# Performance work log

Measured on AMD Instinct MI355X. Metric: run time of the kernel, lower is better.

The kernel has to match this reference:

```python
import jax, jax.numpy as jnp
import numpy as np

B, N, E, H, HEADS = 4, 10000, 160000, 128, 4
NEG_SLOPE = 0.2  # PyG GATConv default
LN_EPS = 1e-5


def setup_inputs() -> dict:
    key = jax.random.key(0)
    ks = jax.random.split(key, 24)
    inp = {}
    inp["node_embeddings"] = jax.random.normal(ks[0], (B, N, H), dtype=jnp.float32)
    inp["src_index"] = jax.random.randint(ks[1], (B, E), 0, N)
    inp["tgt_index"] = jax.random.randint(ks[2], (B, E), 0, N)
    sc = 1.0 / np.sqrt(H)
    for i in range(3):
        j = 3 + 3 * i
        inp[f"W{i+1}"] = jax.random.normal(ks[j], (H, HEADS * H), dtype=jnp.float32) * sc
        inp[f"att_src{i+1}"] = jax.random.normal(ks[j + 1], (HEADS, H), dtype=jnp.float32) * sc
        inp[f"att_dst{i+1}"] = jax.random.normal(ks[j + 2], (HEADS, H), dtype=jnp.float32) * sc
        inp[f"bias{i+1}"] = jnp.zeros((H,), dtype=jnp.float32)
    inp["ln1_g"] = jnp.ones((H,), dtype=jnp.float32)
    inp["ln1_b"] = jnp.zeros((H,), dtype=jnp.float32)
    inp["ln2_g"] = jnp.ones((H,), dtype=jnp.float32)
    inp["ln2_b"] = jnp.zeros((H,), dtype=jnp.float32)
    return inp


def _layer_norm(x, g, b):
    mu = jnp.mean(x, axis=-1, keepdims=True)
    var = jnp.mean((x - mu) ** 2, axis=-1, keepdims=True)
    return (x - mu) * jax.lax.rsqrt(var + LN_EPS) * g + b


def _gat(x, src, tgt, W, a_s, a_d, b):
    # x: [N, H]; src/tgt: [E'] (self-loops already appended). eval mode -> no dropout.
    h = (x @ W).reshape(N, HEADS, H)               # [N, heads, H]
    e_src = jnp.einsum('nhc,hc->nh', h, a_s)       # [N, heads]
    e_dst = jnp.einsum('nhc,hc->nh', h, a_d)
    e = jax.nn.leaky_relu(e_src[src] + e_dst[tgt], NEG_SLOPE)  # [E', heads]
    m = jax.ops.segment_max(e, tgt, num_segments=N)            # per-target max
    ex = jnp.exp(e - m[tgt])
    s = jax.ops.segment_sum(ex, tgt, num_segments=N)
    alpha = ex / s[tgt]                                        # [E', heads]
    out = jax.ops.segment_sum(alpha[:, :, None] * h[src], tgt, num_segments=N)
    return out.mean(axis=1) + b                                # concat=False -> head mean


def reference(node_embeddings, src_index, tgt_index,
              W1, att_src1, att_dst1, bias1,
              W2, att_src2, att_dst2, bias2,
              W3, att_src3, att_dst3, bias3,
              ln1_g, ln1_b, ln2_g, ln2_b):
    loop = jnp.arange(N, dtype=src_index.dtype)

    def one_graph(x, src, tgt):
        s = jnp.concatenate([src, loop])   # GATConv add_self_loops=True (default)
        t = jnp.concatenate([tgt, loop])
        m = _gat(x, s, t, W1, att_src1, att_dst1, bias1)
        m = jax.nn.relu(_layer_norm(m, ln1_g, ln1_b))
        m = _gat(m, s, t, W2, att_src2, att_dst2, bias2)
        m = jax.nn.relu(_layer_norm(m, ln2_g, ln2_b))
        m = _gat(m, s, t, W3, att_src3, att_dst3, bias3)
        return m

    return jax.vmap(one_graph)(node_embeddings, src_index, tgt_index)
```

## Files before the change

kernel.cpp:

```cpp
#include <hip/hip_runtime.h>
#include <hip/hip_bf16.h>
#include <cstdint>
#include <cstddef>

#define B_ 4
#define N_ 10000
#define E_ 160000
#define H_ 128
#define HEADS_ 4
#define HH_ 512
#define NROWS (B_*N_)

typedef __attribute__((ext_vector_type(8))) short bf16x8;
typedef __attribute__((ext_vector_type(4))) float f32x4;
typedef __attribute__((ext_vector_type(2))) float f32x2;

__device__ __forceinline__ float lrelu(float x){ return x > 0.f ? x : 0.2f*x; }
__device__ __forceinline__ unsigned short f2b(float f){
  unsigned int u = __builtin_bit_cast(unsigned int, f);
  unsigned int r = (u + 0x7fffu + ((u >> 16) & 1u)) >> 16;
  return (unsigned short)r;
}
__device__ __forceinline__ float blo(unsigned int u){ return __builtin_bit_cast(float, u << 16); }
__device__ __forceinline__ float bhi(unsigned int u){ return __builtin_bit_cast(float, u & 0xffff0000u); }

__global__ void k_count(const int* __restrict__ tgt, int* __restrict__ cnt){
  int e = blockIdx.x*blockDim.x + threadIdx.x;
  int b = blockIdx.y;
  int t = tgt[(size_t)b*E_ + e];
  atomicAdd(&cnt[b*N_ + t], 1);
}

__global__ void k_scan(const int* __restrict__ cnt, int* __restrict__ off, int* __restrict__ cursor){
  int b = blockIdx.x;
  __shared__ int wsum[16];
  __shared__ int carry_s;
  int lane = threadIdx.x & 63, wid = threadIdx.x >> 6;
  if (threadIdx.x == 0){ carry_s = 0; off[b*(N_+1)] = 0; }
  __syncthreads();
  for (int base = 0; base < N_; base += 1024){
    int i = base + threadIdx.x;
    int v = (i < N_) ? cnt[b*N_ + i] : 0;
    int x = v;
    #pragma unroll
    for (int d = 1; d < 64; d <<= 1){
      int y = __shfl_up(x, d);
      if (lane >= d) x += y;
    }
    if (lane == 63) wsum[wid] = x;
    __syncthreads();
    if (wid == 0 && lane < 16){
      int w = wsum[lane];
      #pragma unroll
      for (int d = 1; d < 16; d <<= 1){
        int y = __shfl_up(w, d, 16);
        if (lane >= d) w += y;
      }
      wsum[lane] = w;
    }
    __syncthreads();
    int excl = (wid ? wsum[wid-1] : 0) + carry_s;
    if (i < N_){
      int inc = x + excl;
      off[b*(N_+1) + i + 1] = inc;
      cursor[b*N_ + i] = inc - v;
    }
    __syncthreads();
    if (threadIdx.x == 0) carry_s += wsum[15];
    __syncthreads();
  }
}

__global__ void k_scatter(const int* __restrict__ src, const int* __restrict__ tgt,
                          int* __restrict__ cursor, int* __restrict__ csr){
  int e = blockIdx.x*blockDim.x + threadIdx.x;
  int b = blockIdx.y;
  int t = tgt[(size_t)b*E_ + e];
  int pos = atomicAdd(&cursor[b*N_ + t], 1);
  csr[(size_t)b*E_ + pos] = src[(size_t)b*E_ + e];
}

__global__ void k_prep(const float* __restrict__ W0, const float* __restrict__ W1, const float* __restrict__ W2,
                       const float* __restrict__ as0, const float* __restrict__ as1, const float* __restrict__ as2,
                       const float* __restrict__ ad0, const float* __restrict__ ad1, const float* __restrict__ ad2,
                       float* __restrict__ wasA, float* __restrict__ wadA, unsigned short* __restrict__ wtA){
  int l = blockIdx.y;
  const float* W   = (l==0)?W0:(l==1)?W1:W2;
  const float* asp = (l==0)?as0:(l==1)?as1:as2;
  const float* adp = (l==0)?ad0:(l==1)?ad1:ad2;
  if (blockIdx.x < 256){
    int i = blockIdx.x*256 + threadIdx.x;
    int c = i >> 7, k = i & 127;
    wtA[(size_t)l*HH_*H_ + i] = f2b(W[(size_t)k*HH_ + c]);
  } else {
    int j = (blockIdx.x - 256)*256 + threadIdx.x;
    if (j < H_*HEADS_){
      int k = j >> 2, h = j & 3;
      const float* wrow = W + (size_t)k*HH_ + h*H_;
      const float* asr = asp + h*H_;
      const float* adr = adp + h*H_;
      float ss = 0.f, sd = 0.f;
      for (int c = 0; c < H_; ++c){ float w = wrow[c]; ss += w*asr[c]; sd += w*adr[c]; }
      wasA[l*HH_ + j] = ss; wadA[l*HH_ + j] = sd;
    }
  }
}

__global__ __launch_bounds__(256) void k_cast_logits(const float* __restrict__ X,
    const float* __restrict__ was, const float* __restrict__ wad,
    unsigned short* __restrict__ Xb, float* __restrict__ es, float* __restrict__ ed){
  int gw = (blockIdx.x*blockDim.x + threadIdx.x) >> 6;
  int lane = threadIdx.x & 63;
  float2 v = *(const float2*)(X + (size_t)gw*H_ + lane*2);
  unsigned int o = ((unsigned int)f2b(v.y) << 16) | (unsigned int)f2b(v.x);
  *(unsigned int*)(Xb + (size_t)gw*H_ + lane*2) = o;
  int c = lane*2;
  const f32x4* w4 = (const f32x4*)was;
  const f32x4* d4 = (const f32x4*)wad;
  f32x4 se = v.x*w4[c] + v.y*w4[c+1];
  f32x4 de = v.x*d4[c] + v.y*d4[c+1];
  #pragma unroll
  for (int d = 1; d < 64; d <<= 1){
    se.x += __shfl_xor(se.x,d); se.y += __shfl_xor(se.y,d);
    se.z += __shfl_xor(se.z,d); se.w += __shfl_xor(se.w,d);
    de.x += __shfl_xor(de.x,d); de.y += __shfl_xor(de.y,d);
    de.z += __shfl_xor(de.z,d); de.w += __shfl_xor(de.w,d);
  }
  if (lane == 0){
    *(float4*)(es + (size_t)gw*4) = make_float4(se.x, se.y, se.z, se.w);
    *(float4*)(ed + (size_t)gw*4) = make_float4(de.x, de.y, de.z, de.w);
  }
}

__global__ __launch_bounds__(256) void k_logits(const unsigned short* __restrict__ Xb,
    const float* __restrict__ was, const float* __restrict__ wad,
    float* __restrict__ es, float* __restrict__ ed){
  int gw = (blockIdx.x * blockDim.x + threadIdx.x) >> 6;
  int lane = threadIdx.x & 63;
  unsigned int u = *(const unsigned int*)(Xb + (size_t)gw*H_ + lane*2);
  float xlo = blo(u), xhi = bhi(u);
  int c = lane*2;
  const f32x4* w4 = (const f32x4*)was;
  const f32x4* d4 = (const f32x4*)wad;
  f32x4 se = xlo*w4[c] + xhi*w4[c+1];
  f32x4 de = xlo*d4[c] + xhi*d4[c+1];
  #pragma unroll
  for (int d = 1; d < 64; d <<= 1){
    se.x += __shfl_xor(se.x,d); se.y += __shfl_xor(se.y,d);
    se.z += __shfl_xor(se.z,d); se.w += __shfl_xor(se.w,d);
    de.x += __shfl_xor(de.x,d); de.y += __shfl_xor(de.y,d);
    de.z += __shfl_xor(de.z,d); de.w += __shfl_xor(de.w,d);
  }
  if (lane == 0){
    *(float4*)(es + (size_t)gw*4) = make_float4(se.x, se.y, se.z, se.w);
    *(float4*)(ed + (size_t)gw*4) = make_float4(de.x, de.y, de.z, de.w);
  }
}

__global__ __launch_bounds__(256) void k_gemm_mfma(const unsigned short* __restrict__ Xb,
    const unsigned short* __restrict__ Wt, unsigned short* __restrict__ Hb){
  __shared__ unsigned short xs[64*128];
  __shared__ unsigned short ws[64*128];
  int row0 = blockIdx.x * 64, col0 = blockIdx.y * 64;
  int tid = threadIdx.x;
  int ch = tid & 15, r0 = tid >> 4;
  #pragma unroll
  for (int p = 0; p < 4; ++p){
    int r = r0 + p*16;
    int sc = ch ^ (r & 7);
    *(uint4*)(&xs[r*128 + sc*8]) = *(const uint4*)(Xb + (size_t)(row0 + r)*H_ + ch*8);
    *(uint4*)(&ws[r*128 + sc*8]) = *(const uint4*)(Wt + (size_t)(col0 + r)*H_ + ch*8);
  }
  __syncthreads();
  int w = tid >> 6, l = tid & 63;
  int lr = l & 15, q = l >> 4;
  f32x4 z = {0.f, 0.f, 0.f, 0.f};
  f32x4 acc[4] = {z, z, z, z};
  int arow = w*16 + lr;
  #pragma unroll
  for (int kf = 0; kf < 4; ++kf){
    int bch = kf*4 + q;
    bf16x8 a = *(const bf16x8*)(&xs[arow*128 + (bch ^ (arow & 7))*8]);
    #pragma unroll
    for (int cf = 0; cf < 4; ++cf){
      int brow = cf*16 + lr;
      bf16x8 bfr = *(const bf16x8*)(&ws[brow*128 + (bch ^ (brow & 7))*8]);
      acc[cf] = __builtin_amdgcn_mfma_f32_16x16x32_bf16(a, bfr, acc[cf], 0, 0, 0);
    }
  }
  #pragma unroll
  for (int cf = 0; cf < 4; ++cf){
    #pragma unroll
    for (int rg = 0; rg < 4; ++rg){
      int row = row0 + w*16 + q*4 + rg;
      int col = col0 + cf*16 + lr;
      Hb[(size_t)row*HH_ + col] = f2b(acc[cf][rg]);
    }
  }
}

__global__ __launch_bounds__(256) void k_aggregate(const unsigned short* __restrict__ Hb,
    const float* __restrict__ es, const float* __restrict__ ed,
    const int* __restrict__ off, const int* __restrict__ csr,
    const float* __restrict__ bias, float* __restrict__ Y){
  int gw = (blockIdx.x * blockDim.x + threadIdx.x) >> 6;
  int lane = threadIdx.x & 63;
  int b = gw / N_;
  int t = gw - b*N_;
  const float4 edv = *(const float4*)(ed + (size_t)gw*4);
  int start = off[b*(N_+1) + t];
  int deg = off[b*(N_+1) + t + 1] - start;
  const int* lst = csr + (size_t)b*E_ + start;

  float m0=-1e30f, m1=-1e30f, m2=-1e30f, m3=-1e30f;
  float s0=0.f, s1=0.f, s2=0.f, s3=0.f;
  for (int i = lane; i <= deg; i += 64){
    int srcn = (i < deg) ? lst[i] : t;
    float4 ev = *(const float4*)(es + (size_t)(b*N_ + srcn)*4);
    float e0 = lrelu(ev.x + edv.x);
    float e1 = lrelu(ev.y + edv.y);
    float e2 = lrelu(ev.z + edv.z);
    float e3 = lrelu(ev.w + edv.w);
    float nm;
    nm = fmaxf(m0, e0); s0 = s0*__expf(m0-nm) + __expf(e0-nm); m0 = nm;
    nm = fmaxf(m1, e1); s1 = s1*__expf(m1-nm) + __expf(e1-nm); m1 = nm;
    nm = fmaxf(m2, e2); s2 = s2*__expf(m2-nm) + __expf(e2-nm); m2 = nm;
    nm = fmaxf(m3, e3); s3 = s3*__expf(m3-nm) + __expf(e3-nm); m3 = nm;
  }
  #pragma unroll
  for (int d = 1; d < 64; d <<= 1){
    float om, os, nm;
    om = __shfl_xor(m0, d); os = __shfl_xor(s0, d); nm = fmaxf(m0, om);
    s0 = s0*__expf(m0-nm) + os*__expf(om-nm); m0 = nm;
    om = __shfl_xor(m1, d); os = __shfl_xor(s1, d); nm = fmaxf(m1, om);
    s1 = s1*__expf(m1-nm) + os*__expf(om-nm); m1 = nm;
    om = __shfl_xor(m2, d); os = __shfl_xor(s2, d); nm = fmaxf(m2, om);
    s2 = s2*__expf(m2-nm) + os*__expf(om-nm); m2 = nm;
    om = __shfl_xor(m3, d); os = __shfl_xor(s3, d); nm = fmaxf(m3, om);
    s3 = s3*__expf(m3-nm) + os*__expf(om-nm); m3 = nm;
  }

  int head = lane >> 4;
  float mh, sh, edh;
  if      (head == 0){ mh = m0; sh = s0; edh = edv.x; }
  else if (head == 1){ mh = m1; sh = s1; edh = edv.y; }
  else if (head == 2){ mh = m2; sh = s2; edh = edv.z; }
  else               { mh = m3; sh = s3; edh = edv.w; }
  float rh = 1.0f / sh;
  int cb = head*H_ + (lane & 15)*8;
  const unsigned short* hbase = Hb + (size_t)b*N_*HH_;
  const float* esb = es + (size_t)b*N_*4;
  float a[8] = {0.f,0.f,0.f,0.f,0.f,0.f,0.f,0.f};
  int total = deg + 1;
  int i = 0;
  for (; i + 1 < total; i += 2){
    int sA = lst[i];
    int sB = (i + 1 < deg) ? lst[i+1] : t;
    float eA = esb[(size_t)sA*4 + head];
    float eB = esb[(size_t)sB*4 + head];
    uint4 hA = *(const uint4*)(hbase + (size_t)sA*HH_ + cb);
    uint4 hB = *(const uint4*)(hbase + (size_t)sB*HH_ + cb);
    float aA = __expf(lrelu(eA + edh) - mh) * rh;
    float aB = __expf(lrelu(eB + edh) - mh) * rh;
    a[0] += aA*blo(hA.x); a[1] += aA*bhi(hA.x);
    a[2] += aA*blo(hA.y); a[3] += aA*bhi(hA.y);
    a[4] += aA*blo(hA.z); a[5] += aA*bhi(hA.z);
    a[6] += aA*blo(hA.w); a[7] += aA*bhi(hA.w);
    a[0] += aB*blo(hB.x); a[1] += aB*bhi(hB.x);
    a[2] += aB*blo(hB.y); a[3] += aB*bhi(hB.y);
    a[4] += aB*blo(hB.z); a[5] += aB*bhi(hB.z);
    a[6] += aB*blo(hB.w); a[7] += aB*bhi(hB.w);
  }
  if (i < total){
    int sA = (i < deg) ? lst[i] : t;
    float eA = esb[(size_t)sA*4 + head];
    uint4 hA = *(const uint4*)(hbase + (size_t)sA*HH_ + cb);
    float aA = __expf(lrelu(eA + edh) - mh) * rh;
    a[0] += aA*blo(hA.x); a[1] += aA*bhi(hA.x);
    a[2] += aA*blo(hA.y); a[3] += aA*bhi(hA.y);
    a[4] += aA*blo(hA.z); a[5] += aA*bhi(hA.z);
    a[6] += aA*blo(hA.w); a[7] += aA*bhi(hA.w);
  }
  #pragma unroll
  for (int d = 16; d < 64; d <<= 1)
    #pragma unroll
    for (int j = 0; j < 8; j++) a[j] += __shfl_xor(a[j], d);
  if (lane < 16){
    int c = lane*8;
    float4 o0 = make_float4(0.25f*a[0]+bias[c+0], 0.25f*a[1]+bias[c+1],
                            0.25f*a[2]+bias[c+2], 0.25f*a[3]+bias[c+3]);
    float4 o1 = make_float4(0.25f*a[4]+bias[c+4], 0.25f*a[5]+bias[c+5],
                            0.25f*a[6]+bias[c+6], 0.25f*a[7]+bias[c+7]);
    *(float4*)(Y + (size_t)gw*H_ + c)     = o0;
    *(float4*)(Y + (size_t)gw*H_ + c + 4) = o1;
  }
}

__global__ __launch_bounds__(256) void k_lnrelu(const float* __restrict__ Y,
    const float* __restrict__ g, const float* __restrict__ bb, unsigned short* __restrict__ Xb){
  int gw = (blockIdx.x*blockDim.x + threadIdx.x) >> 6;
  int lane = threadIdx.x & 63;
  float2 v = *(const float2*)(Y + (size_t)gw*H_ + lane*2);
  float sum = v.x + v.y;
  #pragma unroll
  for (int d = 1; d < 64; d <<= 1) sum += __shfl_xor(sum, d);
  float mu = sum * (1.f/H_);
  float dx = v.x - mu, dy = v.y - mu;
  float vs = dx*dx + dy*dy;
  #pragma unroll
  for (int d = 1; d < 64; d <<= 1) vs += __shfl_xor(vs, d);
  float inv = rsqrtf(vs*(1.f/H_) + 1e-5f);
  float2 gv = *(const float2*)(g + lane*2);
  float2 bv = *(const float2*)(bb + lane*2);
  float ox = fmaxf(dx*inv*gv.x + bv.x, 0.f);
  float oy = fmaxf(dy*inv*gv.y + bv.y, 0.f);
  unsigned int o = ((unsigned int)f2b(oy) << 16) | (unsigned int)f2b(ox);
  *(unsigned int*)(Xb + (size_t)gw*H_ + lane*2) = o;
}

extern "C" void kernel_launch(void* const* d_in, const int* in_sizes, int n_in,
                              void* d_out, int out_size, void* d_ws, size_t ws_size,
                              hipStream_t stream){
  const float* x0   = (const float*)d_in[0];
  const int*   srcI = (const int*)d_in[1];
  const int*   tgtI = (const int*)d_in[2];
  const float* Wl[3]  = {(const float*)d_in[3], (const float*)d_in[7],  (const float*)d_in[11]};
  const float* asl[3] = {(const float*)d_in[4], (const float*)d_in[8],  (const float*)d_in[12]};
  const float* adl[3] = {(const float*)d_in[5], (const float*)d_in[9],  (const float*)d_in[13]};
  const float* bl[3]  = {(const float*)d_in[6], (const float*)d_in[10], (const float*)d_in[14]};
  const float* lng[2] = {(const float*)d_in[15], (const float*)d_in[17]};
  const float* lnb[2] = {(const float*)d_in[16], (const float*)d_in[18]};

  char* p = (char*)d_ws;
  auto carve = [&](size_t bytes) -> void* {
    void* r = (void*)p; p += (bytes + 255) & ~(size_t)255; return r;
  };
  int*   off    = (int*)carve((size_t)B_*(N_+1)*4);
  int*   cnt    = (int*)carve((size_t)B_*N_*4);
  int*   cursor = (int*)carve((size_t)B_*N_*4);
  int*   csr    = (int*)carve((size_t)B_*E_*4);
  float* es     = (float*)carve((size_t)NROWS*4*4);
  float* ed     = (float*)carve((size_t)NROWS*4*4);
  float* wasA   = (float*)carve((size_t)3*HH_*4);
  float* wadA   = (float*)carve((size_t)3*HH_*4);
  unsigned short* wtA  = (unsigned short*)carve((size_t)3*HH_*H_*2);
  unsigned short* hbuf = (unsigned short*)carve((size_t)NROWS*HH_*2);
  unsigned short* xbf  = (unsigned short*)carve((size_t)NROWS*H_*2);
  float* tbuf   = (float*)carve((size_t)NROWS*H_*4);

  hipMemsetAsync(cnt, 0, (size_t)B_*N_*4, stream);
  k_count  <<<dim3(E_/256, B_), 256, 0, stream>>>(tgtI, cnt);
  k_scan   <<<B_, 1024, 0, stream>>>(cnt, off, cursor);
  k_scatter<<<dim3(E_/256, B_), 256, 0, stream>>>(srcI, tgtI, cursor, csr);
  k_prep   <<<dim3(258, 3), 256, 0, stream>>>(Wl[0], Wl[1], Wl[2],
                                              asl[0], asl[1], asl[2],
                                              adl[0], adl[1], adl[2],
                                              wasA, wadA, wtA);
  k_cast_logits<<<NROWS/4, 256, 0, stream>>>(x0, wasA, wadA, xbf, es, ed);

  for (int l = 0; l < 3; ++l){
    k_gemm_mfma<<<dim3(NROWS/64, HH_/64), 256, 0, stream>>>(xbf, wtA + (size_t)l*HH_*H_, hbuf);
    float* yout = (l == 2) ? (float*)d_out : tbuf;
    k_aggregate<<<NROWS/4, 256, 0, stream>>>(hbuf, es, ed, off, csr, bl[l], yout);
    if (l < 2){
      k_lnrelu<<<NROWS/4, 256, 0, stream>>>(tbuf, lng[l], lnb[l], xbf);
      k_logits<<<NROWS/4, 256, 0, stream>>>(xbf, wasA + (size_t)(l+1)*HH_, wadA + (size_t)(l+1)*HH_, es, ed);
    }
  }
}
```

Baseline: 484.3 us.

## Map graphs to XCD pairs and stream all GEMM columns per row block

Block indices in the GEMM and aggregate kernels are remapped so that each graph's work is spread round-robin over a fixed pair of XCDs. The intent is for the per-graph H buffer and logits gathered by the aggregate kernel to stay local to those XCDs' L2 caches. The GEMM now has each block load its 64-row A tile once, keep the fragments in registers, and loop over all 512 output columns with double-buffered W tiles in shared memory. That trades a larger grid for fewer A reloads, but adds a barrier per column chunk and guards for the ragged last row tile.

```diff
diff --git a/kernel.cpp b/kernel.cpp
--- a/kernel.cpp
+++ b/kernel.cpp
@@ -160,42 +160,69 @@
 __global__ __launch_bounds__(256) void k_gemm_mfma(const unsigned short* __restrict__ Xb,
     const unsigned short* __restrict__ Wt, unsigned short* __restrict__ Hb){
   __shared__ unsigned short xs[64*128];
-  __shared__ unsigned short ws[64*128];
-  int row0 = blockIdx.x * 64, col0 = blockIdx.y * 64;
+  __shared__ unsigned short ws[2][64*128];
+  int idx = blockIdx.x;
+  int g = (idx & 7) >> 1;
+  int j = ((idx >> 3) << 1) | (idx & 1);
+  if (j >= 157) return;
+  int rmax = N_ - j*64; if (rmax > 64) rmax = 64;
+  size_t row0 = (size_t)g*N_ + (size_t)j*64;
   int tid = threadIdx.x;
   int ch = tid & 15, r0 = tid >> 4;
   #pragma unroll
   for (int p = 0; p < 4; ++p){
     int r = r0 + p*16;
+    int rr = (r < rmax) ? r : 0;
     int sc = ch ^ (r & 7);
-    *(uint4*)(&xs[r*128 + sc*8]) = *(const uint4*)(Xb + (size_t)(row0 + r)*H_ + ch*8);
-    *(uint4*)(&ws[r*128 + sc*8]) = *(const uint4*)(Wt + (size_t)(col0 + r)*H_ + ch*8);
+    *(uint4*)(&xs[r*128 + sc*8]) = *(const uint4*)(Xb + (row0 + rr)*H_ + ch*8);
+    *(uint4*)(&ws[0][r*128 + sc*8]) = *(const uint4*)(Wt + (size_t)r*H_ + ch*8);
   }
   __syncthreads();
   int w = tid >> 6, l = tid & 63;
   int lr = l & 15, q = l >> 4;
-  f32x4 z = {0.f, 0.f, 0.f, 0.f};
-  f32x4 acc[4] = {z, z, z, z};
   int arow = w*16 + lr;
+  bf16x8 afr[4];
   #pragma unroll
   for (int kf = 0; kf < 4; ++kf){
     int bch = kf*4 + q;
-    bf16x8 a = *(const bf16x8*)(&xs[arow*128 + (bch ^ (arow & 7))*8]);
+    afr[kf] = *(const bf16x8*)(&xs[arow*128 + (bch ^ (arow & 7))*8]);
+  }
+  #pragma unroll
+  for (int cbk = 0; cbk < 8; ++cbk){
+    int cur = cbk & 1;
+    if (cbk < 7){
+      #pragma unroll
+      for (int p = 0; p < 4; ++p){
+        int r = r0 + p*16;
+        int sc = ch ^ (r & 7);
+        *(uint4*)(&ws[cur^1][r*128 + sc*8]) =
+            *(const uint4*)(Wt + (size_t)((cbk+1)*64 + r)*H_ + ch*8);
+      }
+    }
+    f32x4 z = {0.f, 0.f, 0.f, 0.f};
+    f32x4 acc[4] = {z, z, z, z};
+    #pragma unroll
+    for (int kf = 0; kf < 4; ++kf){
+      int bch = kf*4 + q;
+      #pragma unroll
+      for (int cf = 0; cf < 4; ++cf){
+        int brow = cf*16 + lr;
+        bf16x8 bfr = *(const bf16x8*)(&ws[cur][brow*128 + (bch ^ (brow & 7))*8]);
+        acc[cf] = __builtin_amdgcn_mfma_f32_16x16x32_bf16(afr[kf], bfr, acc[cf], 0, 0, 0);
+      }
+    }
     #pragma unroll
     for (int cf = 0; cf < 4; ++cf){
-      int brow = cf*16 + lr;
-      bf16x8 bfr = *(const bf16x8*)(&ws[brow*128 + (bch ^ (brow & 7))*8]);
-      acc[cf] = __builtin_amdgcn_mfma_f32_16x16x32_bf16(a, bfr, acc[cf], 0, 0, 0);
-    }
-  }
-  #pragma unroll
-  for (int cf = 0; cf < 4; ++cf){
-    #pragma unroll
-    for (int rg = 0; rg < 4; ++rg){
-      int row = row0 + w*16 + q*4 + rg;
-      int col = col0 + cf*16 + lr;
-      Hb[(size_t)row*HH_ + col] = f2b(acc[cf][rg]);
-    }
+      #pragma unroll
+      for (int rg = 0; rg < 4; ++rg){
+        int rloc = w*16 + q*4 + rg;
+        if (rloc < rmax){
+          int col = cbk*64 + cf*16 + lr;
+          Hb[(row0 + rloc)*HH_ + col] = f2b(acc[cf][rg]);
+        }
+      }
+    }
+    __syncthreads();
   }
 }
 
@@ -203,10 +230,12 @@
     const float* __restrict__ es, const float* __restrict__ ed,
     const int* __restrict__ off, const int* __restrict__ csr,
     const float* __restrict__ bias, float* __restrict__ Y){
-  int gw = (blockIdx.x * blockDim.x + threadIdx.x) >> 6;
+  int idx = blockIdx.x;
+  int b = (idx & 7) >> 1;
+  int j = ((idx >> 3) << 1) | (idx & 1);
   int lane = threadIdx.x & 63;
-  int b = gw / N_;
-  int t = gw - b*N_;
+  int t = j*4 + (threadIdx.x >> 6);
+  int gw = b*N_ + t;
   const float4 edv = *(const float4*)(ed + (size_t)gw*4);
   int start = off[b*(N_+1) + t];
   int deg = off[b*(N_+1) + t + 1] - start;
@@ -284,7 +313,7 @@
   #pragma unroll
   for (int d = 16; d < 64; d <<= 1)
     #pragma unroll
-    for (int j = 0; j < 8; j++) a[j] += __shfl_xor(a[j], d);
+    for (int j2 = 0; j2 < 8; j2++) a[j2] += __shfl_xor(a[j2], d);
   if (lane < 16){
     int c = lane*8;
     float4 o0 = make_float4(0.25f*a[0]+bias[c+0], 0.25f*a[1]+bias[c+1],
@@ -359,7 +388,7 @@
   k_cast_logits<<<NROWS/4, 256, 0, stream>>>(x0, wasA, wadA, xbf, es, ed);
 
   for (int l = 0; l < 3; ++l){
-    k_gemm_mfma<<<dim3(NROWS/64, HH_/64), 256, 0, stream>>>(xbf, wtA + (size_t)l*HH_*H_, hbuf);
+    k_gemm_mfma<<<632, 256, 0, stream>>>(xbf, wtA + (size_t)l*HH_*H_, hbuf);
     float* yout = (l == 2) ? (float*)d_out : tbuf;
     k_aggregate<<<NROWS/4, 256, 0, stream>>>(hbuf, es, ed, off, csr, bl[l], yout);
     if (l < 2){
```

Measured after the change: 456.3 us. 1.06x faster.
